# Performance work log

Hardware: AMD Instinct MI355X
Metric: run time of the kernel (lower is better)

The kernel has to match this reference:

```python
import jax, jax.numpy as jnp
import numpy as np

H = 16  # num_heads


def setup_inputs() -> dict:
    key = jax.random.key(0)
    k1, k2, k3, k4, k5, k6 = jax.random.split(key, 6)
    B, T, K = 4, 2048, 1024
    x = jax.random.normal(k1, (B, T, K), dtype=jnp.float32)
    s = 1.0 / np.sqrt(K)
    Wq = jax.random.normal(k2, (K, K), dtype=jnp.float32) * s
    Wk = jax.random.normal(k3, (K, K), dtype=jnp.float32) * s
    Wv = jax.random.normal(k4, (K, K), dtype=jnp.float32) * s
    Wp = jax.random.normal(k5, (K, K), dtype=jnp.float32) * s
    bp = jax.random.normal(k6, (K,), dtype=jnp.float32) * 0.01
    return {"input_data": x, "Wq": Wq, "Wk": Wk, "Wv": Wv, "Wp": Wp, "bp": bp}


def reference(input_data, Wq, Wk, Wv, Wp, bp):
    B, T, K = input_data.shape
    S = K // H
    # torch Linear: y = x @ W.T
    q = (input_data @ Wq.T).reshape(B, T, H, S).transpose(0, 2, 1, 3)  # [B,H,T,S]
    k = (input_data @ Wk.T).reshape(B, T, H, S).transpose(0, 2, 1, 3)
    v = (input_data @ Wv.T).reshape(B, T, H, S).transpose(0, 2, 1, 3)
    scale = float(H) ** -0.5  # NB: original scales by num_heads**-0.5, not head_dim
    wei = jnp.einsum("bhts,bhus->bhtu", q, k) * scale  # [B,H,T,T]
    causal = jnp.tril(jnp.ones((T, T), dtype=bool))
    wei = jnp.where(causal, wei, -jnp.inf)
    wei = jax.nn.softmax(wei, axis=-1)
    out = jnp.einsum("bhtu,bhus->bhts", wei, v)  # [B,H,T,S]
    out = out.transpose(0, 2, 1, 3).reshape(B, T, K)
    return out @ Wp.T + bp
```

## Files before the change

kernel.cpp:

```cpp
#include <hip/hip_runtime.h>
#include <hip/hip_bf16.h>
#include <math.h>

typedef __bf16 bf16;
typedef __bf16 bf16x8 __attribute__((ext_vector_type(8)));
typedef float f32x4 __attribute__((ext_vector_type(4)));

#define MFMA16(a, b, c) __builtin_amdgcn_mfma_f32_16x16x32_bf16(a, b, c, 0, 0, 0)

__device__ __forceinline__ void gload16(const void* g, void* l) {
    __builtin_amdgcn_global_load_lds(
        (const __attribute__((address_space(1))) void*)g,
        (__attribute__((address_space(3))) void*)l, 16, 0, 0);
}

__global__ void cast_f32_bf16(const float* __restrict__ src, bf16* __restrict__ dst, int n8) {
    int i = blockIdx.x * blockDim.x + threadIdx.x;
    if (i >= n8) return;
    const float4* s = (const float4*)src;
    float4 v0 = s[i * 2], v1 = s[i * 2 + 1];
    bf16x8 o;
    o[0] = (bf16)v0.x; o[1] = (bf16)v0.y; o[2] = (bf16)v0.z; o[3] = (bf16)v0.w;
    o[4] = (bf16)v1.x; o[5] = (bf16)v1.y; o[6] = (bf16)v1.z; o[7] = (bf16)v1.w;
    *(bf16x8*)(dst + i * 8) = o;
}

__global__ void cast_weights(const float* __restrict__ Wq, const float* __restrict__ Wk,
                             const float* __restrict__ Wv, const float* __restrict__ Wp,
                             bf16* __restrict__ wqkv, bf16* __restrict__ wp) {
    int c = blockIdx.x * blockDim.x + threadIdx.x;
    int mat = c >> 17, loc = c & 131071;
    const float* src = (mat == 0) ? Wq : (mat == 1) ? Wk : (mat == 2) ? Wv : Wp;
    bf16* dst = (mat == 3) ? wp : (wqkv + (size_t)mat * 1048576);
    const float4* s = (const float4*)(src) + loc * 2;
    float4 v0 = s[0], v1 = s[1];
    bf16x8 o;
    o[0] = (bf16)v0.x; o[1] = (bf16)v0.y; o[2] = (bf16)v0.z; o[3] = (bf16)v0.w;
    o[4] = (bf16)v1.x; o[5] = (bf16)v1.y; o[6] = (bf16)v1.z; o[7] = (bf16)v1.w;
    *(bf16x8*)(dst + (size_t)loc * 8) = o;
}

__device__ __forceinline__ void gemm_mainloop(
    const bf16* __restrict__ A, const bf16* __restrict__ W,
    int tm, int tn, int K, bf16* As, bf16* Bs,
    f32x4 acc[4][4], int lane, int wave, int wr, int wc) {
    for (int k0 = 0; k0 < K; k0 += 64) {
#pragma unroll
        for (int it = 0; it < 4; ++it) {
            int o = it * 4096 + wave * 1024 + lane * 16;
            int L = o ^ (((o >> 7) & 7) << 4);
            int row = L >> 7, colb = L & 127;
            gload16((const char*)A + ((size_t)(tm + row) * K + k0) * 2 + colb,
                    (char*)As + it * 4096 + wave * 1024);
            gload16((const char*)W + ((size_t)(tn + row) * K + k0) * 2 + colb,
                    (char*)Bs + it * 4096 + wave * 1024);
        }
        __syncthreads();
#pragma unroll
        for (int kk = 0; kk < 64; kk += 32) {
            bf16x8 a[4], b[4];
#pragma unroll
            for (int i = 0; i < 4; ++i) {
                int row = wr * 64 + i * 16 + (lane & 15);
                int byte = (row * 128 + kk * 2 + ((lane >> 4) * 16)) ^ ((row & 7) << 4);
                a[i] = *(const bf16x8*)((const char*)As + byte);
            }
#pragma unroll
            for (int j = 0; j < 4; ++j) {
                int row = wc * 64 + j * 16 + (lane & 15);
                int byte = (row * 128 + kk * 2 + ((lane >> 4) * 16)) ^ ((row & 7) << 4);
                b[j] = *(const bf16x8*)((const char*)Bs + byte);
            }
#pragma unroll
            for (int i = 0; i < 4; ++i)
#pragma unroll
                for (int j = 0; j < 4; ++j)
                    acc[i][j] = MFMA16(a[i], b[j], acc[i][j]);
        }
        __syncthreads();
    }
}

__global__ void gemm_qkv(const bf16* __restrict__ A, const bf16* __restrict__ W,
                         bf16* __restrict__ qkv) {
    __shared__ bf16 SM[128 * 128];
    bf16* As = SM;
    bf16* Bs = SM + 8192;
    const int tid = threadIdx.x;
    const int lane = tid & 63, wave = tid >> 6;
    const int wr = wave >> 1, wc = wave & 1;
    const int l15 = lane & 15, hi = lane >> 4;
    const int tm = blockIdx.y * 128, tn = blockIdx.x * 128;
    f32x4 acc[4][4] = {};
    gemm_mainloop(A, W, tm, tn, 1024, As, Bs, acc, lane, wave, wr, wc);
    const int mat = tn >> 10;
    if (mat == 2) {
#pragma unroll
        for (int i = 0; i < 4; ++i)
#pragma unroll
            for (int r = 0; r < 4; ++r) {
                int tl = wr * 64 + i * 16 + hi * 4 + r;
#pragma unroll
                for (int j = 0; j < 4; ++j) {
                    int c = wc * 64 + j * 16 + l15;
                    int byte = (c * 256 + tl * 2) ^ ((c & 7) << 4);
                    *(bf16*)((char*)SM + byte) = (bf16)acc[i][j][r];
                }
            }
        __syncthreads();
        const int b16 = (tm >> 11) * 16, tmod = tm & 2047;
#pragma unroll
        for (int pass = 0; pass < 8; ++pass) {
            int c = (tid >> 4) + pass * 16;
            int h = ((tn + c) >> 6) & 15, s = c & 63;
            int byte = (c * 256 + (tid & 15) * 16) ^ ((c & 7) << 4);
            bf16x8 v = *(const bf16x8*)((const char*)SM + byte);
            size_t base = (size_t)(128 + b16 + h) * 131072 + (size_t)s * 2048 + tmod;
            *(bf16x8*)(qkv + base + (tid & 15) * 8) = v;
        }
    } else {
        const float scale = (mat == 0) ? 0.25f : 1.0f;
#pragma unroll
        for (int i = 0; i < 4; ++i)
#pragma unroll
            for (int r = 0; r < 4; ++r) {
                int m = tm + wr * 64 + i * 16 + hi * 4 + r;
                int b_ = m >> 11, t = m & 2047;
#pragma unroll
                for (int j = 0; j < 4; ++j) {
                    int n = tn + wc * 64 + j * 16 + l15;
                    int h = (n >> 6) & 15, s = n & 63;
                    qkv[(size_t)(mat * 64 + b_ * 16 + h) * 131072 + (size_t)t * 64 + s] =
                        (bf16)(acc[i][j][r] * scale);
                }
            }
    }
}

__global__ void gemm_out(const bf16* __restrict__ A, const bf16* __restrict__ W,
                         const float* __restrict__ bias, float* __restrict__ out) {
    __shared__ bf16 As[128 * 64];
    __shared__ bf16 Bs[128 * 64];
    const int lane = threadIdx.x & 63, wave = threadIdx.x >> 6;
    const int wr = wave >> 1, wc = wave & 1;
    const int tm = blockIdx.y * 128, tn = blockIdx.x * 128;
    f32x4 acc[4][4] = {};
    gemm_mainloop(A, W, tm, tn, 1024, As, Bs, acc, lane, wave, wr, wc);
#pragma unroll
    for (int i = 0; i < 4; ++i)
#pragma unroll
        for (int r = 0; r < 4; ++r) {
            int m = tm + wr * 64 + i * 16 + (lane >> 4) * 4 + r;
#pragma unroll
            for (int j = 0; j < 4; ++j) {
                int n = tn + wc * 64 + j * 16 + (lane & 15);
                out[(size_t)m * 1024 + n] = acc[i][j][r] + bias[n];
            }
        }
}

__global__ __launch_bounds__(256, 4)
void attn_kernel(const bf16* __restrict__ qkv, bf16* __restrict__ attn_out) {
    const int wgid = blockIdx.x;
    const int qp = (wgid >> 3) & 15;
    const int bh = ((wgid & 7) << 3) | (wgid >> 7);
    const int tid = threadIdx.x;
    const int lane = tid & 63, wave = tid >> 6;
    const int l15 = lane & 15, hi = lane >> 4;
    const bf16* Qp = qkv + (size_t)bh * 131072;
    const bf16* Kp = qkv + (size_t)(64 + bh) * 131072;
    const bf16* Vt = qkv + (size_t)(128 + bh) * 131072;

    __shared__ bf16 KsBuf[2][4096];
    __shared__ bf16 VsBuf[2][4096];
    __shared__ bf16 PsBuf[4096];

    int k_off[2], vt_off[2];
#pragma unroll
    for (int c = 0; c < 2; ++c) {
        int i = c * 256 + tid;
        int o = i * 16;
        int row = i >> 3;
        int colb = (o ^ ((row & 7) << 4)) & 127;
        k_off[c]  = row * 128  + colb;
        vt_off[c] = row * 4096 + colb;
    }

    const int b_ = bh >> 4, h = bh & 15;

    for (int pass = 0; pass < 2; ++pass) {
        const int qi = pass ? (31 - qp) : qp;
        bf16x8 qf[2];
        {
            int row = qi * 64 + wave * 16 + l15;
#pragma unroll
            for (int ks = 0; ks < 2; ++ks)
                qf[ks] = *(const bf16x8*)(Qp + (size_t)row * 64 + ks * 32 + hi * 8);
        }
        f32x4 o_acc[4] = {};
        float l_run[4] = {0.f, 0.f, 0.f, 0.f};

        const int nkt = qi + 1;
        __syncthreads();
#pragma unroll
        for (int c = 0; c < 2; ++c) {
            gload16((const char*)Kp + k_off[c], (char*)KsBuf[0] + c * 4096 + wave * 1024);
            gload16((const char*)Vt + vt_off[c], (char*)VsBuf[0] + c * 4096 + wave * 1024);
        }
        int cur = 0;
        for (int kt = 0; kt < nkt; ++kt) {
            __syncthreads();
            if (kt + 1 < nkt) {
                size_t kof = (size_t)(kt + 1) * 8192;
                size_t vof = (size_t)(kt + 1) * 128;
#pragma unroll
                for (int c = 0; c < 2; ++c) {
                    gload16((const char*)Kp + kof + k_off[c],
                            (char*)KsBuf[cur ^ 1] + c * 4096 + wave * 1024);
                    gload16((const char*)Vt + vof + vt_off[c],
                            (char*)VsBuf[cur ^ 1] + c * 4096 + wave * 1024);
                }
            }

            const char* Ks = (const char*)KsBuf[cur];
            const char* Vs = (const char*)VsBuf[cur];
            f32x4 sc[4] = {};
#pragma unroll
            for (int ks = 0; ks < 2; ++ks)
#pragma unroll
                for (int kf = 0; kf < 4; ++kf) {
                    int row = kf * 16 + l15;
                    int byte = (row * 128 + ks * 64 + hi * 16) ^ ((row & 7) << 4);
                    bf16x8 kb = *(const bf16x8*)(Ks + byte);
                    sc[kf] = MFMA16(qf[ks], kb, sc[kf]);
                }

            if (kt == qi) {
#pragma unroll
                for (int r = 0; r < 4; ++r) {
                    int row_g = qi * 64 + wave * 16 + hi * 4 + r;
#pragma unroll
                    for (int kf = 0; kf < 4; ++kf) {
                        int key_g = kt * 64 + kf * 16 + l15;
                        float p = (key_g > row_g) ? 0.f : __expf(sc[kf][r]);
                        sc[kf][r] = p;
                        l_run[r] += p;
                    }
                }
            } else {
#pragma unroll
                for (int r = 0; r < 4; ++r)
#pragma unroll
                    for (int kf = 0; kf < 4; ++kf) {
                        float p = __expf(sc[kf][r]);
                        sc[kf][r] = p;
                        l_run[r] += p;
                    }
            }

#pragma unroll
            for (int kf = 0; kf < 4; ++kf)
#pragma unroll
                for (int r = 0; r < 4; ++r) {
                    int row = wave * 16 + hi * 4 + r;
                    int byte = (row * 128 + (kf * 16 + l15) * 2) ^ (((row >> 1) & 7) << 4);
                    *(bf16*)((char*)PsBuf + byte) = (bf16)sc[kf][r];
                }
            asm volatile("s_waitcnt lgkmcnt(0)" ::: "memory");
            __builtin_amdgcn_sched_barrier(0);

#pragma unroll
            for (int ks = 0; ks < 2; ++ks) {
                int prow = wave * 16 + l15;
                int pbyte = (prow * 128 + ks * 64 + hi * 16) ^ (((prow >> 1) & 7) << 4);
                bf16x8 pa = *(const bf16x8*)((const char*)PsBuf + pbyte);
#pragma unroll
                for (int sf = 0; sf < 4; ++sf) {
                    int srow = sf * 16 + l15;
                    int vbyte = (srow * 128 + ks * 64 + hi * 16) ^ ((srow & 7) << 4);
                    bf16x8 vb = *(const bf16x8*)(Vs + vbyte);
                    o_acc[sf] = MFMA16(pa, vb, o_acc[sf]);
                }
            }
            cur ^= 1;
        }

#pragma unroll
        for (int r = 0; r < 4; ++r) {
            float l = l_run[r];
#pragma unroll
            for (int mk = 1; mk < 16; mk <<= 1)
                l += __shfl_xor(l, mk, 64);
            float inv = 1.0f / l;
            int t = qi * 64 + wave * 16 + hi * 4 + r;
            size_t base = ((size_t)(b_ * 2048 + t)) * 1024 + h * 64;
#pragma unroll
            for (int sf = 0; sf < 4; ++sf)
                attn_out[base + sf * 16 + l15] = (bf16)(o_acc[sf][r] * inv);
        }
    }
}

extern "C" void kernel_launch(void* const* d_in, const int* in_sizes, int n_in,
                              void* d_out, int out_size, void* d_ws, size_t ws_size,
                              hipStream_t stream) {
    const float* x  = (const float*)d_in[0];
    const float* Wq = (const float*)d_in[1];
    const float* Wk = (const float*)d_in[2];
    const float* Wv = (const float*)d_in[3];
    const float* Wp = (const float*)d_in[4];
    const float* bp = (const float*)d_in[5];
    float* out = (float*)d_out;

    char* ws = (char*)d_ws;
    bf16* x_bf   = (bf16*)(ws);
    bf16* wqkv   = (bf16*)(ws + 16777216);
    bf16* wp_bf  = (bf16*)(ws + 23068672);
    bf16* qkv    = (bf16*)(ws + 25165824);
    bf16* attn_b = (bf16*)(ws + 75497472);

    cast_f32_bf16<<<dim3(4096), 256, 0, stream>>>(x, x_bf, 8192 * 1024 / 8);
    cast_weights<<<dim3(2048), 256, 0, stream>>>(Wq, Wk, Wv, Wp, wqkv, wp_bf);

    gemm_qkv<<<dim3(24, 64), 256, 0, stream>>>(x_bf, wqkv, qkv);
    attn_kernel<<<dim3(1024), 256, 0, stream>>>(qkv, attn_b);
    gemm_out<<<dim3(8, 64), 256, 0, stream>>>(attn_b, wp_bf, bp, out);
}
```

Measured before the change: 159.4 us.

## Double attention query tile per workgroup to 128 rows, halving grid

Each attention workgroup now handles a 128-row query tile, with each wave owning two 16-row fragments, instead of a 64-row tile. Every K/V tile loaded into LDS is therefore reused for twice as many queries, which halves K/V global and LDS traffic per query and gives more MFMAs per barrier. The costs are a grid of 512 workgroups instead of 1024, higher register pressure, a doubled P buffer in LDS, and coarser causal masking on the last two key tiles, which wastes some compute.

```diff
diff --git a/kernel.cpp b/kernel.cpp
--- a/kernel.cpp
+++ b/kernel.cpp
@@ -162,8 +162,8 @@
 __global__ __launch_bounds__(256, 4)
 void attn_kernel(const bf16* __restrict__ qkv, bf16* __restrict__ attn_out) {
     const int wgid = blockIdx.x;
-    const int qp = (wgid >> 3) & 15;
-    const int bh = ((wgid & 7) << 3) | (wgid >> 7);
+    const int qp = (wgid >> 3) & 7;
+    const int bh = ((wgid & 7) << 3) | (wgid >> 6);
     const int tid = threadIdx.x;
     const int lane = tid & 63, wave = tid >> 6;
     const int l15 = lane & 15, hi = lane >> 4;
@@ -173,7 +173,7 @@
 
     __shared__ bf16 KsBuf[2][4096];
     __shared__ bf16 VsBuf[2][4096];
-    __shared__ bf16 PsBuf[4096];
+    __shared__ bf16 PsBuf[8192];
 
     int k_off[2], vt_off[2];
 #pragma unroll
@@ -189,18 +189,19 @@
     const int b_ = bh >> 4, h = bh & 15;
 
     for (int pass = 0; pass < 2; ++pass) {
-        const int qi = pass ? (31 - qp) : qp;
-        bf16x8 qf[2];
-        {
-            int row = qi * 64 + wave * 16 + l15;
+        const int qi = pass ? (15 - qp) : qp;
+        bf16x8 qf[2][2];
+#pragma unroll
+        for (int rf = 0; rf < 2; ++rf) {
+            int row = qi * 128 + wave * 32 + rf * 16 + l15;
 #pragma unroll
             for (int ks = 0; ks < 2; ++ks)
-                qf[ks] = *(const bf16x8*)(Qp + (size_t)row * 64 + ks * 32 + hi * 8);
-        }
-        f32x4 o_acc[4] = {};
-        float l_run[4] = {0.f, 0.f, 0.f, 0.f};
-
-        const int nkt = qi + 1;
+                qf[rf][ks] = *(const bf16x8*)(Qp + (size_t)row * 64 + ks * 32 + hi * 8);
+        }
+        f32x4 o_acc[2][4] = {};
+        float l_run[2][4] = {};
+
+        const int nkt = 2 * qi + 2;
         __syncthreads();
 #pragma unroll
         for (int c = 0; c < 2; ++c) {
@@ -224,7 +225,7 @@
 
             const char* Ks = (const char*)KsBuf[cur];
             const char* Vs = (const char*)VsBuf[cur];
-            f32x4 sc[4] = {};
+            f32x4 sc[2][4] = {};
 #pragma unroll
             for (int ks = 0; ks < 2; ++ks)
 #pragma unroll
@@ -232,72 +233,88 @@
                     int row = kf * 16 + l15;
                     int byte = (row * 128 + ks * 64 + hi * 16) ^ ((row & 7) << 4);
                     bf16x8 kb = *(const bf16x8*)(Ks + byte);
-                    sc[kf] = MFMA16(qf[ks], kb, sc[kf]);
-                }
-
-            if (kt == qi) {
-#pragma unroll
-                for (int r = 0; r < 4; ++r) {
-                    int row_g = qi * 64 + wave * 16 + hi * 4 + r;
-#pragma unroll
-                    for (int kf = 0; kf < 4; ++kf) {
-                        int key_g = kt * 64 + kf * 16 + l15;
-                        float p = (key_g > row_g) ? 0.f : __expf(sc[kf][r]);
-                        sc[kf][r] = p;
-                        l_run[r] += p;
+#pragma unroll
+                    for (int rf = 0; rf < 2; ++rf)
+                        sc[rf][kf] = MFMA16(qf[rf][ks], kb, sc[rf][kf]);
+                }
+
+            if (kt >= 2 * qi) {
+#pragma unroll
+                for (int rf = 0; rf < 2; ++rf)
+#pragma unroll
+                    for (int r = 0; r < 4; ++r) {
+                        int row_g = qi * 128 + wave * 32 + rf * 16 + hi * 4 + r;
+#pragma unroll
+                        for (int kf = 0; kf < 4; ++kf) {
+                            int key_g = kt * 64 + kf * 16 + l15;
+                            float p = (key_g > row_g) ? 0.f : __expf(sc[rf][kf][r]);
+                            sc[rf][kf][r] = p;
+                            l_run[rf][r] += p;
+                        }
                     }
-                }
             } else {
 #pragma unroll
-                for (int r = 0; r < 4; ++r)
-#pragma unroll
-                    for (int kf = 0; kf < 4; ++kf) {
-                        float p = __expf(sc[kf][r]);
-                        sc[kf][r] = p;
-                        l_run[r] += p;
+                for (int rf = 0; rf < 2; ++rf)
+#pragma unroll
+                    for (int r = 0; r < 4; ++r)
+#pragma unroll
+                        for (int kf = 0; kf < 4; ++kf) {
+                            float p = __expf(sc[rf][kf][r]);
+                            sc[rf][kf][r] = p;
+                            l_run[rf][r] += p;
+                        }
+            }
+
+#pragma unroll
+            for (int rf = 0; rf < 2; ++rf)
+#pragma unroll
+                for (int kf = 0; kf < 4; ++kf)
+#pragma unroll
+                    for (int r = 0; r < 4; ++r) {
+                        int row = wave * 32 + rf * 16 + hi * 4 + r;
+                        int byte = (row * 128 + (kf * 16 + l15) * 2) ^ (((row >> 1) & 7) << 4);
+                        *(bf16*)((char*)PsBuf + byte) = (bf16)sc[rf][kf][r];
                     }
-            }
-
-#pragma unroll
-            for (int kf = 0; kf < 4; ++kf)
-#pragma unroll
-                for (int r = 0; r < 4; ++r) {
-                    int row = wave * 16 + hi * 4 + r;
-                    int byte = (row * 128 + (kf * 16 + l15) * 2) ^ (((row >> 1) & 7) << 4);
-                    *(bf16*)((char*)PsBuf + byte) = (bf16)sc[kf][r];
-                }
             asm volatile("s_waitcnt lgkmcnt(0)" ::: "memory");
             __builtin_amdgcn_sched_barrier(0);
 
 #pragma unroll
             for (int ks = 0; ks < 2; ++ks) {
-                int prow = wave * 16 + l15;
-                int pbyte = (prow * 128 + ks * 64 + hi * 16) ^ (((prow >> 1) & 7) << 4);
-                bf16x8 pa = *(const bf16x8*)((const char*)PsBuf + pbyte);
+                bf16x8 pa[2];
+#pragma unroll
+                for (int rf = 0; rf < 2; ++rf) {
+                    int prow = wave * 32 + rf * 16 + l15;
+                    int pbyte = (prow * 128 + ks * 64 + hi * 16) ^ (((prow >> 1) & 7) << 4);
+                    pa[rf] = *(const bf16x8*)((const char*)PsBuf + pbyte);
+                }
 #pragma unroll
                 for (int sf = 0; sf < 4; ++sf) {
                     int srow = sf * 16 + l15;
                     int vbyte = (srow * 128 + ks * 64 + hi * 16) ^ ((srow & 7) << 4);
                     bf16x8 vb = *(const bf16x8*)(Vs + vbyte);
-                    o_acc[sf] = MFMA16(pa, vb, o_acc[sf]);
+#pragma unroll
+                    for (int rf = 0; rf < 2; ++rf)
+                        o_acc[rf][sf] = MFMA16(pa[rf], vb, o_acc[rf][sf]);
                 }
             }
             cur ^= 1;
         }
 
 #pragma unroll
-        for (int r = 0; r < 4; ++r) {
-            float l = l_run[r];
-#pragma unroll
-            for (int mk = 1; mk < 16; mk <<= 1)
-                l += __shfl_xor(l, mk, 64);
-            float inv = 1.0f / l;
-            int t = qi * 64 + wave * 16 + hi * 4 + r;
-            size_t base = ((size_t)(b_ * 2048 + t)) * 1024 + h * 64;
-#pragma unroll
-            for (int sf = 0; sf < 4; ++sf)
-                attn_out[base + sf * 16 + l15] = (bf16)(o_acc[sf][r] * inv);
-        }
+        for (int rf = 0; rf < 2; ++rf)
+#pragma unroll
+            for (int r = 0; r < 4; ++r) {
+                float l = l_run[rf][r];
+#pragma unroll
+                for (int mk = 1; mk < 16; mk <<= 1)
+                    l += __shfl_xor(l, mk, 64);
+                float inv = 1.0f / l;
+                int t = qi * 128 + wave * 32 + rf * 16 + hi * 4 + r;
+                size_t base = ((size_t)(b_ * 2048 + t)) * 1024 + h * 64;
+#pragma unroll
+                for (int sf = 0; sf < 4; ++sf)
+                    attn_out[base + sf * 16 + l15] = (bf16)(o_acc[rf][sf][r] * inv);
+            }
     }
 }
 
@@ -323,6 +340,6 @@
     cast_weights<<<dim3(2048), 256, 0, stream>>>(Wq, Wk, Wv, Wp, wqkv, wp_bf);
 
     gemm_qkv<<<dim3(24, 64), 256, 0, stream>>>(x_bf, wqkv, qkv);
-    attn_kernel<<<dim3(1024), 256, 0, stream>>>(qkv, attn_b);
+    attn_kernel<<<dim3(512), 256, 0, stream>>>(qkv, attn_b);
     gemm_out<<<dim3(8, 64), 256, 0, stream>>>(attn_b, wp_bf, bp, out);
 }
```

Measured after the change: 160.1 us. No clear change (+0.5%).
